# Performance work log

Hardware: AMD Instinct MI355X
Metric: run time of the kernel (lower is better)

The kernel has to match this reference:

```python
import jax, jax.numpy as jnp
import numpy as np

B, G, O, N, T = 32, 16, 256, 88, 256


def setup_inputs() -> dict:
    key = jax.random.key(0)
    k1, k2, k3, k4, k5 = jax.random.split(key, 5)
    x = jax.random.normal(k1, (B, N, T), dtype=jnp.float32)
    y = jax.random.uniform(k2, (B, G), dtype=jnp.float32)  # soft genre weights
    weight = jax.random.normal(k3, (G, O, N, T), dtype=jnp.float32) * 0.05
    mask = (jax.random.uniform(k4, (O, T)) < 0.5).astype(jnp.float32)
    bias = jax.random.normal(k5, (O,), dtype=jnp.float32)
    return {"x": x, "y": y, "weight": weight, "mask": mask, "bias": bias}


def reference(x, y, weight, mask, bias):
    # Original: maskedWeight = einsum('gont,ot->gont'); genreWeight = einsum('bg,gont->bont');
    # out = einsum('bnt,bont->bno') + bias. Fused into one contraction (same math,
    # avoids materializing the [b,o,n,t] intermediate).
    out = jnp.einsum('bnt,bg,gont,ot->bno', x, y, weight, mask)
    return out + bias
```

## Files before the change

kernel.cpp:

```cpp
#include <hip/hip_runtime.h>

#define Bq 32
#define Gq 16
#define Oq 256
#define Nq 88
#define Tq 256

typedef short bf16x8 __attribute__((ext_vector_type(8)));
typedef float f32x4 __attribute__((ext_vector_type(4)));

static __device__ __forceinline__ short f2bf(float f) {
    return __builtin_bit_cast(short, (__bf16)f);
}

static __device__ __forceinline__ void gld_lds16_nt(const float* src, float* lds_dst) {
    __builtin_amdgcn_global_load_lds(
        (const __attribute__((address_space(1))) void*)src,
        (__attribute__((address_space(3))) void*)lds_dst, 16, 0,  18);
}

__global__ __launch_bounds__(256, 3)
void mlm_mfma8(const float* __restrict__ x, const float* __restrict__ y,
               const float* __restrict__ w, const float* __restrict__ mask,
               const float* __restrict__ bias, float* __restrict__ out) {
    __shared__ float wbuf[3][4096];
    __shared__ float y_lds[512];

    const int bid = blockIdx.x;
    const int n  = bid >> 4;
    const int o0 = (bid & 15) << 4;

    const int tid  = threadIdx.x;
    const int wv   = tid >> 6;
    const int lane = tid & 63;
    const int lo = lane & 15;
    const int hi = lane >> 4;
    const int sr = lo & 7;

    y_lds[tid]       = y[tid];
    y_lds[tid + 256] = y[tid + 256];

    bf16x8 afrag[2][2];
    f32x4 mka[2], mkb[2];
    const int tbase = wv * 64;
#pragma unroll
    for (int W = 0; W < 2; ++W) {
        const int ta = tbase + W * 32 + hi * 4;
        const int tb = ta + 16;
        f32x4 xa0 = *(const f32x4*)(x + ((size_t)lo * Nq + n) * Tq + ta);
        f32x4 xb0 = *(const f32x4*)(x + ((size_t)lo * Nq + n) * Tq + tb);
        f32x4 xa1 = *(const f32x4*)(x + ((size_t)(lo + 16) * Nq + n) * Tq + ta);
        f32x4 xb1 = *(const f32x4*)(x + ((size_t)(lo + 16) * Nq + n) * Tq + tb);
        mka[W] = *(const f32x4*)(mask + (size_t)(o0 + lo) * Tq + ta);
        mkb[W] = *(const f32x4*)(mask + (size_t)(o0 + lo) * Tq + tb);
#pragma unroll
        for (int j = 0; j < 4; ++j) {
            afrag[W][0][j]     = f2bf(xa0[j]);
            afrag[W][0][j + 4] = f2bf(xb0[j]);
            afrag[W][1][j]     = f2bf(xa1[j]);
            afrag[W][1][j + 4] = f2bf(xb1[j]);
        }
    }

    const size_t GS = (size_t)Oq * Nq * Tq;
    const float* wsrc[4];
#pragma unroll
    for (int q = 0; q < 4; ++q) {
        const int r = wv * 4 + q;
        wsrc[q] = w + ((size_t)(o0 + r) * Nq + n) * Tq + ((lane ^ (r & 7)) << 2);
    }

    __syncthreads();

#pragma unroll
    for (int q = 0; q < 4; ++q)
        gld_lds16_nt(wsrc[q], &wbuf[0][(wv * 4 + q) * 256]);
#pragma unroll
    for (int q = 0; q < 4; ++q)
        gld_lds16_nt(wsrc[q] + GS, &wbuf[1][(wv * 4 + q) * 256]);
    asm volatile("s_waitcnt vmcnt(4)" ::: "memory");
    __builtin_amdgcn_s_barrier();
    __builtin_amdgcn_sched_barrier(0);

    const float* wpre[4];
#pragma unroll
    for (int q = 0; q < 4; ++q) wpre[q] = wsrc[q] + 2 * GS;

    f32x4 facc0 = {0.f, 0.f, 0.f, 0.f};
    f32x4 facc1 = {0.f, 0.f, 0.f, 0.f};

    int cb = 0;
    int pb = 2;
#pragma unroll 1
    for (int g = 0; g < 16; ++g) {
        if (g < 14) {
#pragma unroll
            for (int q = 0; q < 4; ++q) {
                gld_lds16_nt(wpre[q], &wbuf[pb][(wv * 4 + q) * 256]);
                wpre[q] += GS;
            }
        }

        const float* wrow = &wbuf[cb][lo * 256];
        f32x4 acc0 = {0.f, 0.f, 0.f, 0.f};
        f32x4 acc1 = {0.f, 0.f, 0.f, 0.f};
#pragma unroll
        for (int W = 0; W < 2; ++W) {
            const int c0 = wv * 16 + W * 8 + hi;
            f32x4 wa4 = *(const f32x4*)(wrow + ((c0 ^ sr) << 2));
            f32x4 wb4 = *(const f32x4*)(wrow + (((c0 + 4) ^ sr) << 2));
            bf16x8 bfr;
#pragma unroll
            for (int j = 0; j < 4; ++j) {
                bfr[j]     = f2bf(wa4[j] * mka[W][j]);
                bfr[j + 4] = f2bf(wb4[j] * mkb[W][j]);
            }
            acc0 = __builtin_amdgcn_mfma_f32_16x16x32_bf16(afrag[W][0], bfr, acc0, 0, 0, 0);
            acc1 = __builtin_amdgcn_mfma_f32_16x16x32_bf16(afrag[W][1], bfr, acc1, 0, 0, 0);
        }

#pragma unroll
        for (int i = 0; i < 4; ++i) {
            facc0[i] += y_lds[(hi * 4 + i) * Gq + g] * acc0[i];
            facc1[i] += y_lds[(16 + hi * 4 + i) * Gq + g] * acc1[i];
        }

        if (g < 14) {
            asm volatile("s_waitcnt vmcnt(4)" ::: "memory");
            __builtin_amdgcn_s_barrier();
            __builtin_amdgcn_sched_barrier(0);
        } else if (g == 14) {
            asm volatile("s_waitcnt vmcnt(0)" ::: "memory");
            __builtin_amdgcn_s_barrier();
            __builtin_amdgcn_sched_barrier(0);
        }

        cb = (cb == 2) ? 0 : cb + 1;
        pb = (pb == 2) ? 0 : pb + 1;
    }

    __syncthreads();
    float (*red)[32][16] = (float (*)[32][16]) & wbuf[0][0];
#pragma unroll
    for (int i = 0; i < 4; ++i) {
        red[wv][hi * 4 + i][lo]      = facc0[i];
        red[wv][16 + hi * 4 + i][lo] = facc1[i];
    }
    __syncthreads();

#pragma unroll
    for (int s = 0; s < 2; ++s) {
        const int idx = tid + s * 256;
        const int b  = idx >> 4;
        const int oo = idx & 15;
        const float v = red[0][b][oo] + red[1][b][oo] + red[2][b][oo] + red[3][b][oo]
                      + bias[o0 + oo];
        out[((size_t)b * Nq + n) * Oq + o0 + oo] = v;
    }
}

extern "C" void kernel_launch(void* const* d_in, const int* in_sizes, int n_in,
                              void* d_out, int out_size, void* d_ws, size_t ws_size,
                              hipStream_t stream) {
    const float* x    = (const float*)d_in[0];
    const float* y    = (const float*)d_in[1];
    const float* w    = (const float*)d_in[2];
    const float* mask = (const float*)d_in[3];
    const float* bias = (const float*)d_in[4];
    float* out = (float*)d_out;

    dim3 grid(Nq * (Oq / 16));
    dim3 block(256);
    hipLaunchKernelGGL(mlm_mfma8, grid, block, 0, stream, x, y, w, mask, bias, out);
}
```

Before: 69.88 us.

## Stage weight tiles through registers into double-buffered LDS instead of direct global-to-LDS

Replaces the direct global_load_lds triple-buffered pipeline with nontemporal vector loads into registers, which are then written to a swizzled, double-buffered LDS tile. Two genre slices are held in flight in registers while the other buffer is computed. The g loop is unrolled in pairs. This cuts LDS use from three buffers to two, which could help occupancy, but it adds VGPR pressure and explicit ds_write traffic plus lgkmcnt waits.

```diff
diff --git a/kernel.cpp b/kernel.cpp
--- a/kernel.cpp
+++ b/kernel.cpp
@@ -13,17 +13,11 @@
     return __builtin_bit_cast(short, (__bf16)f);
 }
 
-static __device__ __forceinline__ void gld_lds16_nt(const float* src, float* lds_dst) {
-    __builtin_amdgcn_global_load_lds(
-        (const __attribute__((address_space(1))) void*)src,
-        (__attribute__((address_space(3))) void*)lds_dst, 16, 0,  18);
-}
-
 __global__ __launch_bounds__(256, 3)
-void mlm_mfma8(const float* __restrict__ x, const float* __restrict__ y,
+void mlm_mfma9(const float* __restrict__ x, const float* __restrict__ y,
                const float* __restrict__ w, const float* __restrict__ mask,
                const float* __restrict__ bias, float* __restrict__ out) {
-    __shared__ float wbuf[3][4096];
+    __shared__ float wbuf[2][4096];
     __shared__ float y_lds[512];
 
     const int bid = blockIdx.x;
@@ -63,45 +57,44 @@
     }
 
     const size_t GS = (size_t)Oq * Nq * Tq;
-    const float* wsrc[4];
+    const float* wptr[4];
+    float* dwp[4];
 #pragma unroll
     for (int q = 0; q < 4; ++q) {
         const int r = wv * 4 + q;
-        wsrc[q] = w + ((size_t)(o0 + r) * Nq + n) * Tq + ((lane ^ (r & 7)) << 2);
+        wptr[q] = w + ((size_t)(o0 + r) * Nq + n) * Tq + (lane << 2);
+        dwp[q]  = &wbuf[0][r * 256 + ((lane ^ (r & 7)) << 2)];
     }
 
     __syncthreads();
 
+    f32x4 regA[4], regB[4];
 #pragma unroll
-    for (int q = 0; q < 4; ++q)
-        gld_lds16_nt(wsrc[q], &wbuf[0][(wv * 4 + q) * 256]);
+    for (int q = 0; q < 4; ++q) {
+        regA[q] = __builtin_nontemporal_load((const f32x4*)wptr[q]);
+        wptr[q] += GS;
+    }
 #pragma unroll
-    for (int q = 0; q < 4; ++q)
-        gld_lds16_nt(wsrc[q] + GS, &wbuf[1][(wv * 4 + q) * 256]);
+    for (int q = 0; q < 4; ++q) {
+        regB[q] = __builtin_nontemporal_load((const f32x4*)wptr[q]);
+        wptr[q] += GS;
+    }
     asm volatile("s_waitcnt vmcnt(4)" ::: "memory");
+#pragma unroll
+    for (int q = 0; q < 4; ++q) *(f32x4*)dwp[q] = regA[q];
+#pragma unroll
+    for (int q = 0; q < 4; ++q) {
+        regA[q] = __builtin_nontemporal_load((const f32x4*)wptr[q]);
+        wptr[q] += GS;
+    }
+    asm volatile("s_waitcnt lgkmcnt(0)" ::: "memory");
     __builtin_amdgcn_s_barrier();
     __builtin_amdgcn_sched_barrier(0);
-
-    const float* wpre[4];
-#pragma unroll
-    for (int q = 0; q < 4; ++q) wpre[q] = wsrc[q] + 2 * GS;
 
     f32x4 facc0 = {0.f, 0.f, 0.f, 0.f};
     f32x4 facc1 = {0.f, 0.f, 0.f, 0.f};
 
-    int cb = 0;
-    int pb = 2;
-#pragma unroll 1
-    for (int g = 0; g < 16; ++g) {
-        if (g < 14) {
-#pragma unroll
-            for (int q = 0; q < 4; ++q) {
-                gld_lds16_nt(wpre[q], &wbuf[pb][(wv * 4 + q) * 256]);
-                wpre[q] += GS;
-            }
-        }
-
-        const float* wrow = &wbuf[cb][lo * 256];
+    auto compute_g = [&](int g, const float* wrow) {
         f32x4 acc0 = {0.f, 0.f, 0.f, 0.f};
         f32x4 acc1 = {0.f, 0.f, 0.f, 0.f};
 #pragma unroll
@@ -118,26 +111,55 @@
             acc0 = __builtin_amdgcn_mfma_f32_16x16x32_bf16(afrag[W][0], bfr, acc0, 0, 0, 0);
             acc1 = __builtin_amdgcn_mfma_f32_16x16x32_bf16(afrag[W][1], bfr, acc1, 0, 0, 0);
         }
-
 #pragma unroll
         for (int i = 0; i < 4; ++i) {
             facc0[i] += y_lds[(hi * 4 + i) * Gq + g] * acc0[i];
             facc1[i] += y_lds[(16 + hi * 4 + i) * Gq + g] * acc1[i];
         }
+    };
 
-        if (g < 14) {
-            asm volatile("s_waitcnt vmcnt(4)" ::: "memory");
-            __builtin_amdgcn_s_barrier();
-            __builtin_amdgcn_sched_barrier(0);
-        } else if (g == 14) {
-            asm volatile("s_waitcnt vmcnt(0)" ::: "memory");
-            __builtin_amdgcn_s_barrier();
-            __builtin_amdgcn_sched_barrier(0);
+    const float* wrow0 = &wbuf[0][lo * 256];
+    const float* wrow1 = &wbuf[1][lo * 256];
+
+#pragma unroll 1
+    for (int gp = 0; gp < 7; ++gp) {
+        compute_g(2 * gp, wrow0);
+        asm volatile("s_waitcnt vmcnt(4)" ::: "memory");
+#pragma unroll
+        for (int q = 0; q < 4; ++q) *(f32x4*)(dwp[q] + 4096) = regB[q];
+#pragma unroll
+        for (int q = 0; q < 4; ++q) {
+            regB[q] = __builtin_nontemporal_load((const f32x4*)wptr[q]);
+            wptr[q] += GS;
         }
+        asm volatile("s_waitcnt lgkmcnt(0)" ::: "memory");
+        __builtin_amdgcn_s_barrier();
+        __builtin_amdgcn_sched_barrier(0);
 
-        cb = (cb == 2) ? 0 : cb + 1;
-        pb = (pb == 2) ? 0 : pb + 1;
+        compute_g(2 * gp + 1, wrow1);
+        asm volatile("s_waitcnt vmcnt(4)" ::: "memory");
+#pragma unroll
+        for (int q = 0; q < 4; ++q) *(f32x4*)dwp[q] = regA[q];
+        if (gp < 6) {
+#pragma unroll
+            for (int q = 0; q < 4; ++q) {
+                regA[q] = __builtin_nontemporal_load((const f32x4*)wptr[q]);
+                wptr[q] += GS;
+            }
+        }
+        asm volatile("s_waitcnt lgkmcnt(0)" ::: "memory");
+        __builtin_amdgcn_s_barrier();
+        __builtin_amdgcn_sched_barrier(0);
     }
+
+    compute_g(14, wrow0);
+    asm volatile("s_waitcnt vmcnt(0)" ::: "memory");
+#pragma unroll
+    for (int q = 0; q < 4; ++q) *(f32x4*)(dwp[q] + 4096) = regB[q];
+    asm volatile("s_waitcnt lgkmcnt(0)" ::: "memory");
+    __builtin_amdgcn_s_barrier();
+    __builtin_amdgcn_sched_barrier(0);
+    compute_g(15, wrow1);
 
     __syncthreads();
     float (*red)[32][16] = (float (*)[32][16]) & wbuf[0][0];
@@ -171,5 +193,5 @@
 
     dim3 grid(Nq * (Oq / 16));
     dim3 block(256);
-    hipLaunchKernelGGL(mlm_mfma8, grid, block, 0, stream, x, y, w, mask, bias, out);
+    hipLaunchKernelGGL(mlm_mfma9, grid, block, 0, stream, x, y, w, mask, bias, out);
 }
```

After: 68.73 us. About the same (-1.7%).
